# Kernel optimization log

Measured on AMD Instinct MI355X. Metric: run time of the kernel, lower is better.

Reference implementation:

```python
import jax, jax.numpy as jnp
import numpy as np

K_NEIGHBOURS = 16
ITERATIONS = 3
NUM_CLASSES = 20
N_POINTS = 20000


def setup_inputs() -> dict:
    key = jax.random.key(0)
    k1, k2 = jax.random.split(key)
    logits = jax.random.normal(k1, (N_POINTS, NUM_CLASSES), dtype=jnp.float32)
    coords = jax.random.uniform(k2, (N_POINTS, 3), dtype=jnp.float32)
    # nn.init.eye_ then *= -0.1
    compat_w = (-0.1 * jnp.eye(NUM_CLASSES, dtype=jnp.float32))
    return {"logits": logits, "coords": coords, "compat_w": compat_w}


def _knn_graph(coords, k):
    # torch.cdist (p=2): euclidean distances, (N, N)
    sq = jnp.sum(coords * coords, axis=-1)
    d2 = sq[:, None] + sq[None, :] - 2.0 * (coords @ coords.T)
    dists = jnp.sqrt(jnp.clip(d2, 0.0))
    # smallest-k -> top_k of negated distances
    _, idx = jax.lax.top_k(-dists, k)  # (N, k)
    return idx


def reference(logits, coords, compat_w):
    knn_idx = _knn_graph(coords, K_NEIGHBOURS)
    q = jax.nn.softmax(logits, axis=-1)
    for _ in range(ITERATIONS):
        neighbour_q = q[knn_idx]            # (N, k, K) gather
        msg = jnp.mean(neighbour_q, axis=1)  # (N, K)
        refined = logits + msg @ compat_w.T  # nn.Linear: x @ W^T
        q = jax.nn.softmax(refined, axis=-1)
    return (refined, q)
```

## Files before the change

### kernel.cpp

```cpp
#include <hip/hip_runtime.h>

#define N_PTS 20000
#define NCLS 20
#define KNN 16
#define GRID 12
#define NCELLS (GRID * GRID * GRID)
#define HCELL (1.0f / (float)GRID)
#define CAND_CAP 1152
#define KEY_CAP 192
#define R_TARGET 0.0680f

__device__ __forceinline__ int cell1d(float v) {
    int c = (int)(v * (float)GRID);
    return min(max(c, 0), GRID - 1);
}

__global__ __launch_bounds__(1024) void build_kernel(const float* __restrict__ coords,
                                                     int* __restrict__ cellStart,
                                                     int* __restrict__ cellCursor) {
    __shared__ int hist[NCELLS];
    __shared__ int part[1024];
    const int t = threadIdx.x;
    for (int c = t; c < NCELLS; c += 1024) hist[c] = 0;
    __syncthreads();
    for (int p = t; p < N_PTS; p += 1024) {
        const int cx = cell1d(coords[3 * p + 0]);
        const int cy = cell1d(coords[3 * p + 1]);
        const int cz = cell1d(coords[3 * p + 2]);
        atomicAdd(&hist[(cz * GRID + cy) * GRID + cx], 1);
    }
    __syncthreads();
    const int c0 = 2 * t, c1 = 2 * t + 1;
    const int v0 = (c0 < NCELLS) ? hist[c0] : 0;
    const int v1 = (c1 < NCELLS) ? hist[c1] : 0;
    part[t] = v0 + v1;
    __syncthreads();
    for (int off = 1; off < 1024; off <<= 1) {
        const int v = part[t] + ((t >= off) ? part[t - off] : 0);
        __syncthreads();
        part[t] = v;
        __syncthreads();
    }
    const int excl = (t > 0) ? part[t - 1] : 0;
    if (c0 < NCELLS) { cellStart[c0] = excl;      cellCursor[c0] = excl; }
    if (c1 < NCELLS) { cellStart[c1] = excl + v0; cellCursor[c1] = excl + v0; }
    if (t == 1023) cellStart[NCELLS] = part[1023];
}

__global__ __launch_bounds__(256) void scatter_kernel(const float* __restrict__ coords,
                                                      const float* __restrict__ logits,
                                                      int* __restrict__ cellCursor,
                                                      float4* __restrict__ sortedPts,
                                                      int* __restrict__ orig,
                                                      float* __restrict__ ls,
                                                      float* __restrict__ q0s) {
    const int p = blockIdx.x * blockDim.x + threadIdx.x;
    if (p >= N_PTS) return;
    const float x = coords[3 * p + 0];
    const float y = coords[3 * p + 1];
    const float z = coords[3 * p + 2];
    const int c = (cell1d(z) * GRID + cell1d(y)) * GRID + cell1d(x);
    const int pos = atomicAdd(&cellCursor[c], 1);
    sortedPts[pos] = make_float4(x, y, z, __uint_as_float((unsigned)p));
    orig[pos] = p;
    const float4* l4 = (const float4*)(logits + p * NCLS);
    float v[NCLS];
#pragma unroll
    for (int u = 0; u < 5; ++u) {
        const float4 a = l4[u];
        v[4 * u + 0] = a.x; v[4 * u + 1] = a.y;
        v[4 * u + 2] = a.z; v[4 * u + 3] = a.w;
    }
    float4* d4 = (float4*)(ls + pos * NCLS);
#pragma unroll
    for (int u = 0; u < 5; ++u)
        d4[u] = make_float4(v[4 * u], v[4 * u + 1], v[4 * u + 2], v[4 * u + 3]);
    float mx = v[0];
#pragma unroll
    for (int cc = 1; cc < NCLS; ++cc) mx = fmaxf(mx, v[cc]);
    float sum = 0.f;
#pragma unroll
    for (int cc = 0; cc < NCLS; ++cc) { v[cc] = __expf(v[cc] - mx); sum += v[cc]; }
    const float inv = 1.f / sum;
    float4* q4 = (float4*)(q0s + pos * NCLS);
#pragma unroll
    for (int u = 0; u < 5; ++u)
        q4[u] = make_float4(v[4 * u] * inv, v[4 * u + 1] * inv,
                            v[4 * u + 2] * inv, v[4 * u + 3] * inv);
}

__device__ void knn_ladder(const float4* __restrict__ sortedPts,
                           const int* __restrict__ cellStart,
                           const float4 qp, const int s, int hw,
                           unsigned long long* keys, const int lane,
                           int* __restrict__ knn_out) {
    const unsigned long long laneLt = (1ull << lane) - 1ull;
    const int cx = cell1d(qp.x), cy = cell1d(qp.y), cz = cell1d(qp.z);
    float g = 0.9995f * (float)hw * HCELL;
    float tau = g * g;
    int cnt = 0;
    for (int att = 0; att < 16; ++att) {
        cnt = 0;
        const int xlo = max(cx - hw, 0), xhi = min(cx + hw, GRID - 1);
        const int ylo = max(cy - hw, 0), yhi = min(cy + hw, GRID - 1);
        const int zlo = max(cz - hw, 0), zhi = min(cz + hw, GRID - 1);
        for (int zz = zlo; zz <= zhi; ++zz) {
            for (int yy = ylo; yy <= yhi; ++yy) {
                const int rowc = (zz * GRID + yy) * GRID;
                const int beg = cellStart[rowc + xlo];
                const int end = cellStart[rowc + xhi + 1];
                for (int j0 = beg; j0 < end; j0 += 64) {
                    const int j = j0 + lane;
                    const bool jv = j < end;
                    const float4 pt = sortedPts[jv ? j : beg];
                    const float dx = pt.x - qp.x, dy = pt.y - qp.y, dz = pt.z - qp.z;
                    const float d2 = dx * dx + dy * dy + dz * dz;
                    const bool take = jv && (d2 < tau);
                    const unsigned long long mm = __ballot(take);
                    if (take) {
                        const int pos = cnt + (int)__popcll(mm & laneLt);
                        if (pos < KEY_CAP)
                            keys[pos] = (((unsigned long long)__float_as_uint(d2)) << 32) |
                                        (unsigned long long)(unsigned)j;
                    }
                    cnt += (int)__popcll(mm);
                }
            }
        }
        if (cnt >= KNN && cnt <= KEY_CAP) break;
        if (cnt < KNN) {
            if (hw < GRID - 1) { ++hw; g = 0.9995f * (float)hw * HCELL; tau = g * g; }
            else tau *= 2.5f;
        } else {
            tau *= 0.6f;
        }
    }
    const int m = min(cnt, KEY_CAP);
    const unsigned long long k0 = (lane < m) ? keys[lane] : ~0ull;
    const unsigned long long k1 = (lane + 64 < m) ? keys[lane + 64] : ~0ull;
    const unsigned long long k2 = (lane + 128 < m) ? keys[lane + 128] : ~0ull;
    int r0 = 0, r1 = 0, r2 = 0;
    for (int j = 0; j < m; ++j) {
        const unsigned long long kj = keys[j];
        r0 += (kj < k0); r1 += (kj < k1); r2 += (kj < k2);
    }
    if (lane < m && r0 < KNN)       knn_out[s * KNN + r0] = (int)(unsigned)(k0 & 0xffffffffull);
    if (lane + 64 < m && r1 < KNN)  knn_out[s * KNN + r1] = (int)(unsigned)(k1 & 0xffffffffull);
    if (lane + 128 < m && r2 < KNN) knn_out[s * KNN + r2] = (int)(unsigned)(k2 & 0xffffffffull);
}

__global__ __launch_bounds__(256) void knn_kernel(const float4* __restrict__ sortedPts,
                                                  const int* __restrict__ cellStart,
                                                  int* __restrict__ knn_out) {
    __shared__ float4 cand[CAND_CAP];
    __shared__ unsigned long long keys[4][KEY_CAP];
    const int lane = threadIdx.x & 63;
    const int wave = threadIdx.x >> 6;
    const int c = blockIdx.x;
    const int cz = c / (GRID * GRID);
    const int cy = (c / GRID) % GRID;
    const int cx = c % GRID;
    const int pbeg = cellStart[c];
    const int pend = cellStart[c + 1];
    const int npts = pend - pbeg;
    if (npts <= 0) return;
    const int bd = (cx == 0 || cx == GRID - 1) + (cy == 0 || cy == GRID - 1) +
                   (cz == 0 || cz == GRID - 1);
    const int hs = bd ? 2 : 1;
    const unsigned long long laneLt = (1ull << lane) - 1ull;

    const int xlo = max(cx - hs, 0), xhi = min(cx + hs, GRID - 1);
    const int ylo = max(cy - hs, 0), yhi = min(cy + hs, GRID - 1);
    const int zlo = max(cz - hs, 0), zhi = min(cz + hs, GRID - 1);
    const int ny = yhi - ylo + 1;
    const int nruns = (zhi - zlo + 1) * ny;

    int beg = 0, len = 0;
    if (lane < nruns) {
        const int zz = zlo + lane / ny;
        const int yy = ylo + lane % ny;
        const int rowc = (zz * GRID + yy) * GRID;
        beg = cellStart[rowc + xlo];
        len = cellStart[rowc + xhi + 1] - beg;
    }
    int off = len;
#pragma unroll
    for (int sh = 1; sh < 64; sh <<= 1) {
        const int o = __shfl_up(off, sh, 64);
        if (lane >= sh) off += o;
    }
    const int nc = __shfl(off, 63);
    off -= len;
    const int ownRun = (cz - zlo) * ny + (cy - ylo);
    const int ownOff = __shfl(off, ownRun) + (pbeg - __shfl(beg, ownRun));

    if (nc <= CAND_CAP) {
        for (int r = wave; r < nruns; r += 4) {
            const int rb = __shfl(beg, r);
            const int rl = __shfl(len, r);
            const int ro = __shfl(off, r);
            for (int i = lane; i < rl; i += 64) {
                float4 pt = sortedPts[rb + i];
                pt.w = __uint_as_float((unsigned)(rb + i));
                cand[ro + i] = pt;
            }
        }
    }
    __syncthreads();

    if (nc > CAND_CAP) {
        for (int idx = wave; idx < npts; idx += 4)
            knn_ladder(sortedPts, cellStart, sortedPts[pbeg + idx], pbeg + idx,
                       hs + 1, keys[wave], lane, knn_out);
        return;
    }

    const float taumaxr = 0.9995f * (float)hs * HCELL;
    const float taumax = taumaxr * taumaxr;

    for (int idx = wave; idx < npts; idx += 4) {
        const int s = pbeg + idx;
        const float4 qp = cand[ownOff + idx];
        float r = R_TARGET;
        const float inv2r = 0.5f / r;
        const float fx = (fminf(qp.x + r, 1.f) - fmaxf(qp.x - r, 0.f)) * inv2r;
        const float fy = (fminf(qp.y + r, 1.f) - fmaxf(qp.y - r, 0.f)) * inv2r;
        const float fz = (fminf(qp.z + r, 1.f) - fmaxf(qp.z - r, 0.f)) * inv2r;
        const float f = fmaxf(fx * fy * fz, 0.05f);
        r = R_TARGET * __powf(f, -0.33333334f);
        float tau = fminf(r * r, taumax);
        bool triedMax = (tau >= taumax * 0.999f);

        int cnt = 0;
        bool ok = false;
        for (int att = 0; att < 6 && !ok; ++att) {
            cnt = 0;
            for (int j0 = 0; j0 < nc; j0 += 64) {
                const int j = j0 + lane;
                float d2 = 1e30f;
                unsigned pw = 0;
                if (j < nc) {
                    const float4 pt = cand[j];
                    const float dx = pt.x - qp.x, dy = pt.y - qp.y, dz = pt.z - qp.z;
                    d2 = dx * dx + dy * dy + dz * dz;
                    pw = __float_as_uint(pt.w);
                }
                const bool take = d2 < tau;
                const unsigned long long mm = __ballot(take);
                if (take) {
                    const int pos = cnt + (int)__popcll(mm & laneLt);
                    if (pos < KEY_CAP)
                        keys[wave][pos] =
                            (((unsigned long long)__float_as_uint(d2)) << 32) |
                            (unsigned long long)pw;
                }
                cnt += (int)__popcll(mm);
            }
            if (cnt >= KNN && cnt <= KEY_CAP) ok = true;
            else if (cnt < KNN) {
                if (triedMax) break;
                tau = taumax; triedMax = true;
            } else tau *= 0.6f;
        }
        if (!ok) {
            knn_ladder(sortedPts, cellStart, qp, s, hs + 1, keys[wave], lane, knn_out);
            continue;
        }
        const int m = cnt;
        const unsigned long long k0 = (lane < m) ? keys[wave][lane] : ~0ull;
        const unsigned long long k1 = (lane + 64 < m) ? keys[wave][lane + 64] : ~0ull;
        const unsigned long long k2 = (lane + 128 < m) ? keys[wave][lane + 128] : ~0ull;
        int r0 = 0, r1 = 0, r2 = 0;
        for (int j = 0; j < m; ++j) {
            const unsigned long long kj = keys[wave][j];
            r0 += (kj < k0); r1 += (kj < k1); r2 += (kj < k2);
        }
        if (lane < m && r0 < KNN)       knn_out[s * KNN + r0] = (int)(unsigned)(k0 & 0xffffffffull);
        if (lane + 64 < m && r1 < KNN)  knn_out[s * KNN + r1] = (int)(unsigned)(k1 & 0xffffffffull);
        if (lane + 128 < m && r2 < KNN) knn_out[s * KNN + r2] = (int)(unsigned)(k2 & 0xffffffffull);
    }
}

__global__ __launch_bounds__(256) void crf_iter_kernel(const float* __restrict__ ls,
                                                       const float* __restrict__ W,
                                                       const int* __restrict__ knn,
                                                       const float* __restrict__ qin,
                                                       float* __restrict__ qout,
                                                       const int* __restrict__ orig,
                                                       float* __restrict__ outRef,
                                                       float* __restrict__ outQ) {
    __shared__ float Ws[NCLS * NCLS];
    for (int i = threadIdx.x; i < NCLS * NCLS; i += blockDim.x) Ws[i] = W[i];
    __syncthreads();
    const int t = blockIdx.x * blockDim.x + threadIdx.x;
    const int p = t >> 2;
    const int qtr = t & 3;
    if (p >= N_PTS) return;

    float acc[NCLS];
#pragma unroll
    for (int c = 0; c < NCLS; ++c) acc[c] = 0.f;

    const int4 k4 = ((const int4*)(knn + p * KNN))[qtr];
    const int ids[4] = {k4.x, k4.y, k4.z, k4.w};
#pragma unroll
    for (int u = 0; u < 4; ++u) {
        unsigned id = (unsigned)ids[u];
        if (id >= N_PTS) id = 0;
        const float4* r4 = (const float4*)(qin + id * NCLS);
#pragma unroll
        for (int v = 0; v < 5; ++v) {
            const float4 a = r4[v];
            acc[4 * v + 0] += a.x; acc[4 * v + 1] += a.y;
            acc[4 * v + 2] += a.z; acc[4 * v + 3] += a.w;
        }
    }
#pragma unroll
    for (int c = 0; c < NCLS; ++c) {
        acc[c] += __shfl_xor(acc[c], 1, 64);
        acc[c] += __shfl_xor(acc[c], 2, 64);
        acc[c] *= (1.f / 16.f);
    }

    const int c0 = qtr * 5;
    float ref[5];
#pragma unroll
    for (int i = 0; i < 5; ++i) {
        float s = ls[p * NCLS + c0 + i];
#pragma unroll
        for (int k = 0; k < NCLS; ++k) s += acc[k] * Ws[(c0 + i) * NCLS + k];
        ref[i] = s;
    }

    float mx = ref[0];
#pragma unroll
    for (int i = 1; i < 5; ++i) mx = fmaxf(mx, ref[i]);
    mx = fmaxf(mx, __shfl_xor(mx, 1, 64));
    mx = fmaxf(mx, __shfl_xor(mx, 2, 64));
    float ex[5];
    float ps = 0.f;
#pragma unroll
    for (int i = 0; i < 5; ++i) { ex[i] = __expf(ref[i] - mx); ps += ex[i]; }
    ps += __shfl_xor(ps, 1, 64);
    ps += __shfl_xor(ps, 2, 64);
    const float inv = 1.f / ps;

    if (outRef != nullptr) {
        const int o = orig[p];
#pragma unroll
        for (int i = 0; i < 5; ++i) {
            outRef[o * NCLS + c0 + i] = ref[i];
            outQ[o * NCLS + c0 + i] = ex[i] * inv;
        }
    } else {
#pragma unroll
        for (int i = 0; i < 5; ++i) qout[p * NCLS + c0 + i] = ex[i] * inv;
    }
}

extern "C" void kernel_launch(void* const* d_in, const int* in_sizes, int n_in,
                              void* d_out, int out_size, void* d_ws, size_t ws_size,
                              hipStream_t stream) {
    const float* logits = (const float*)d_in[0];
    const float* coords = (const float*)d_in[1];
    const float* W      = (const float*)d_in[2];
    float* out = (float*)d_out;

    char* ws = (char*)d_ws;
    size_t off = 0;
    int* knn = (int*)(ws + off);              off += (size_t)N_PTS * KNN * 4;
    off = (off + 255) & ~(size_t)255;
    float* ls = (float*)(ws + off);           off += (size_t)N_PTS * NCLS * 4;
    off = (off + 255) & ~(size_t)255;
    float* q0s = (float*)(ws + off);          off += (size_t)N_PTS * NCLS * 4;
    off = (off + 255) & ~(size_t)255;
    float4* sortedPts = (float4*)(ws + off);  off += (size_t)N_PTS * 16;
    off = (off + 255) & ~(size_t)255;
    int* orig = (int*)(ws + off);             off += (size_t)N_PTS * 4;
    off = (off + 255) & ~(size_t)255;
    int* cellStart = (int*)(ws + off);        off += (size_t)(NCELLS + 1) * 4;
    off = (off + 255) & ~(size_t)255;
    int* cellCursor = (int*)(ws + off);
    float* q1s = out + N_PTS * NCLS;

    const int threads = 256;
    const int pblocks = (N_PTS + threads - 1) / threads;
    const int cblocks = (4 * N_PTS + threads - 1) / threads;

    build_kernel<<<1, 1024, 0, stream>>>(coords, cellStart, cellCursor);
    scatter_kernel<<<pblocks, threads, 0, stream>>>(coords, logits, cellCursor,
                                                    sortedPts, orig, ls, q0s);
    knn_kernel<<<NCELLS, threads, 0, stream>>>(sortedPts, cellStart, knn);
    crf_iter_kernel<<<cblocks, threads, 0, stream>>>(ls, W, knn, q0s, q1s, orig,
                                                     nullptr, nullptr);
    crf_iter_kernel<<<cblocks, threads, 0, stream>>>(ls, W, knn, q1s, q0s, orig,
                                                     nullptr, nullptr);
    crf_iter_kernel<<<cblocks, threads, 0, stream>>>(ls, W, knn, q0s, nullptr, orig,
                                                     out, out + N_PTS * NCLS);
}
```

Measured before the change: 136.5 us.

## Parallelize cell histogram, split kNN cells across two blocks, shrink candidate caps

Replaces the single-block histogram and scan with a grid-wide atomic count kernel where the last block to finish does the prefix scan, which removes a serial single-workgroup stage. The kNN kernel now launches two blocks per cell, each handling alternate query points. The candidate neighbourhood is fixed to 3x3x3 cells with smaller shared-memory caps (CAND_CAP 512, KEY_CAP 128), which cuts LDS use and the rank-sort work. The trade-off is that the two blocks per cell duplicate the candidate load, and more queries may fall back to the slower ladder search when a cell's candidate count exceeds the smaller cap or boundary cells lack enough neighbours.

After: 129.7 us. 1.05x faster.

```diff
diff --git a/kernel.cpp b/kernel.cpp
--- a/kernel.cpp
+++ b/kernel.cpp
@@ -6,8 +6,8 @@
 #define GRID 12
 #define NCELLS (GRID * GRID * GRID)
 #define HCELL (1.0f / (float)GRID)
-#define CAND_CAP 1152
-#define KEY_CAP 192
+#define CAND_CAP 512
+#define KEY_CAP 128
 #define R_TARGET 0.0680f
 
 __device__ __forceinline__ int cell1d(float v) {
@@ -15,36 +15,58 @@
     return min(max(c, 0), GRID - 1);
 }
 
-__global__ __launch_bounds__(1024) void build_kernel(const float* __restrict__ coords,
-                                                     int* __restrict__ cellStart,
-                                                     int* __restrict__ cellCursor) {
-    __shared__ int hist[NCELLS];
-    __shared__ int part[1024];
-    const int t = threadIdx.x;
-    for (int c = t; c < NCELLS; c += 1024) hist[c] = 0;
-    __syncthreads();
-    for (int p = t; p < N_PTS; p += 1024) {
+__global__ __launch_bounds__(256) void count_scan_kernel(const float* __restrict__ coords,
+                                                         int* __restrict__ cellCount,
+                                                         int* __restrict__ doneCtr,
+                                                         int* __restrict__ cellStart,
+                                                         int* __restrict__ cellCursor) {
+    const int p = blockIdx.x * blockDim.x + threadIdx.x;
+    if (p < N_PTS) {
         const int cx = cell1d(coords[3 * p + 0]);
         const int cy = cell1d(coords[3 * p + 1]);
         const int cz = cell1d(coords[3 * p + 2]);
-        atomicAdd(&hist[(cz * GRID + cy) * GRID + cx], 1);
-    }
+        atomicAdd(&cellCount[(cz * GRID + cy) * GRID + cx], 1);
+    }
+    __threadfence();
     __syncthreads();
-    const int c0 = 2 * t, c1 = 2 * t + 1;
-    const int v0 = (c0 < NCELLS) ? hist[c0] : 0;
-    const int v1 = (c1 < NCELLS) ? hist[c1] : 0;
-    part[t] = v0 + v1;
+    __shared__ bool isLast;
+    if (threadIdx.x == 0)
+        isLast = (atomicAdd(doneCtr, 1) == (int)gridDim.x - 1);
     __syncthreads();
-    for (int off = 1; off < 1024; off <<= 1) {
+    if (!isLast) return;
+
+    __shared__ int part[256];
+    const int t = threadIdx.x;
+    const int base = t * 7;
+    int local[7];
+    int s = 0;
+#pragma unroll
+    for (int i = 0; i < 7; ++i) {
+        const int c = base + i;
+        const int v = (c < NCELLS)
+            ? __hip_atomic_load(&cellCount[c], __ATOMIC_RELAXED, __HIP_MEMORY_SCOPE_AGENT)
+            : 0;
+        local[i] = s;
+        s += v;
+    }
+    part[t] = s;
+    __syncthreads();
+    for (int off = 1; off < 256; off <<= 1) {
         const int v = part[t] + ((t >= off) ? part[t - off] : 0);
         __syncthreads();
         part[t] = v;
         __syncthreads();
     }
     const int excl = (t > 0) ? part[t - 1] : 0;
-    if (c0 < NCELLS) { cellStart[c0] = excl;      cellCursor[c0] = excl; }
-    if (c1 < NCELLS) { cellStart[c1] = excl + v0; cellCursor[c1] = excl + v0; }
-    if (t == 1023) cellStart[NCELLS] = part[1023];
+#pragma unroll
+    for (int i = 0; i < 7; ++i) {
+        const int c = base + i;
+        if (c < NCELLS) {
+            cellStart[c] = excl + local[i];
+            cellCursor[c] = excl + local[i];
+        }
+    }
+    if (t == 255) cellStart[NCELLS] = part[255];
 }
 
 __global__ __launch_bounds__(256) void scatter_kernel(const float* __restrict__ coords,
@@ -138,15 +160,13 @@
     const int m = min(cnt, KEY_CAP);
     const unsigned long long k0 = (lane < m) ? keys[lane] : ~0ull;
     const unsigned long long k1 = (lane + 64 < m) ? keys[lane + 64] : ~0ull;
-    const unsigned long long k2 = (lane + 128 < m) ? keys[lane + 128] : ~0ull;
-    int r0 = 0, r1 = 0, r2 = 0;
+    int r0 = 0, r1 = 0;
     for (int j = 0; j < m; ++j) {
         const unsigned long long kj = keys[j];
-        r0 += (kj < k0); r1 += (kj < k1); r2 += (kj < k2);
-    }
-    if (lane < m && r0 < KNN)       knn_out[s * KNN + r0] = (int)(unsigned)(k0 & 0xffffffffull);
-    if (lane + 64 < m && r1 < KNN)  knn_out[s * KNN + r1] = (int)(unsigned)(k1 & 0xffffffffull);
-    if (lane + 128 < m && r2 < KNN) knn_out[s * KNN + r2] = (int)(unsigned)(k2 & 0xffffffffull);
+        r0 += (kj < k0); r1 += (kj < k1);
+    }
+    if (lane < m && r0 < KNN)      knn_out[s * KNN + r0] = (int)(unsigned)(k0 & 0xffffffffull);
+    if (lane + 64 < m && r1 < KNN) knn_out[s * KNN + r1] = (int)(unsigned)(k1 & 0xffffffffull);
 }
 
 __global__ __launch_bounds__(256) void knn_kernel(const float4* __restrict__ sortedPts,
@@ -156,7 +176,8 @@
     __shared__ unsigned long long keys[4][KEY_CAP];
     const int lane = threadIdx.x & 63;
     const int wave = threadIdx.x >> 6;
-    const int c = blockIdx.x;
+    const int c = blockIdx.x >> 1;
+    const int half = blockIdx.x & 1;
     const int cz = c / (GRID * GRID);
     const int cy = (c / GRID) % GRID;
     const int cx = c % GRID;
@@ -164,14 +185,11 @@
     const int pend = cellStart[c + 1];
     const int npts = pend - pbeg;
     if (npts <= 0) return;
-    const int bd = (cx == 0 || cx == GRID - 1) + (cy == 0 || cy == GRID - 1) +
-                   (cz == 0 || cz == GRID - 1);
-    const int hs = bd ? 2 : 1;
     const unsigned long long laneLt = (1ull << lane) - 1ull;
 
-    const int xlo = max(cx - hs, 0), xhi = min(cx + hs, GRID - 1);
-    const int ylo = max(cy - hs, 0), yhi = min(cy + hs, GRID - 1);
-    const int zlo = max(cz - hs, 0), zhi = min(cz + hs, GRID - 1);
+    const int xlo = max(cx - 1, 0), xhi = min(cx + 1, GRID - 1);
+    const int ylo = max(cy - 1, 0), yhi = min(cy + 1, GRID - 1);
+    const int zlo = max(cz - 1, 0), zhi = min(cz + 1, GRID - 1);
     const int ny = yhi - ylo + 1;
     const int nruns = (zhi - zlo + 1) * ny;
 
@@ -185,11 +203,11 @@
     }
     int off = len;
 #pragma unroll
-    for (int sh = 1; sh < 64; sh <<= 1) {
+    for (int sh = 1; sh < 16; sh <<= 1) {
         const int o = __shfl_up(off, sh, 64);
         if (lane >= sh) off += o;
     }
-    const int nc = __shfl(off, 63);
+    const int nc = __shfl(off, nruns - 1);
     off -= len;
     const int ownRun = (cz - zlo) * ny + (cy - ylo);
     const int ownOff = __shfl(off, ownRun) + (pbeg - __shfl(beg, ownRun));
@@ -209,16 +227,16 @@
     __syncthreads();
 
     if (nc > CAND_CAP) {
-        for (int idx = wave; idx < npts; idx += 4)
+        for (int idx = 2 * wave + half; idx < npts; idx += 8)
             knn_ladder(sortedPts, cellStart, sortedPts[pbeg + idx], pbeg + idx,
-                       hs + 1, keys[wave], lane, knn_out);
+                       2, keys[wave], lane, knn_out);
         return;
     }
 
-    const float taumaxr = 0.9995f * (float)hs * HCELL;
+    const float taumaxr = 0.9995f * HCELL;
     const float taumax = taumaxr * taumaxr;
 
-    for (int idx = wave; idx < npts; idx += 4) {
+    for (int idx = 2 * wave + half; idx < npts; idx += 8) {
         const int s = pbeg + idx;
         const float4 qp = cand[ownOff + idx];
         float r = R_TARGET;
@@ -233,7 +251,7 @@
 
         int cnt = 0;
         bool ok = false;
-        for (int att = 0; att < 6 && !ok; ++att) {
+        for (int att = 0; att < 5 && !ok; ++att) {
             cnt = 0;
             for (int j0 = 0; j0 < nc; j0 += 64) {
                 const int j = j0 + lane;
@@ -263,21 +281,19 @@
             } else tau *= 0.6f;
         }
         if (!ok) {
-            knn_ladder(sortedPts, cellStart, qp, s, hs + 1, keys[wave], lane, knn_out);
+            knn_ladder(sortedPts, cellStart, qp, s, 2, keys[wave], lane, knn_out);
             continue;
         }
         const int m = cnt;
         const unsigned long long k0 = (lane < m) ? keys[wave][lane] : ~0ull;
         const unsigned long long k1 = (lane + 64 < m) ? keys[wave][lane + 64] : ~0ull;
-        const unsigned long long k2 = (lane + 128 < m) ? keys[wave][lane + 128] : ~0ull;
-        int r0 = 0, r1 = 0, r2 = 0;
+        int r0 = 0, r1 = 0;
         for (int j = 0; j < m; ++j) {
             const unsigned long long kj = keys[wave][j];
-            r0 += (kj < k0); r1 += (kj < k1); r2 += (kj < k2);
-        }
-        if (lane < m && r0 < KNN)       knn_out[s * KNN + r0] = (int)(unsigned)(k0 & 0xffffffffull);
-        if (lane + 64 < m && r1 < KNN)  knn_out[s * KNN + r1] = (int)(unsigned)(k1 & 0xffffffffull);
-        if (lane + 128 < m && r2 < KNN) knn_out[s * KNN + r2] = (int)(unsigned)(k2 & 0xffffffffull);
+            r0 += (kj < k0); r1 += (kj < k1);
+        }
+        if (lane < m && r0 < KNN)      knn_out[s * KNN + r0] = (int)(unsigned)(k0 & 0xffffffffull);
+        if (lane + 64 < m && r1 < KNN) knn_out[s * KNN + r1] = (int)(unsigned)(k1 & 0xffffffffull);
     }
 }
 
@@ -378,6 +394,9 @@
     off = (off + 255) & ~(size_t)255;
     int* orig = (int*)(ws + off);             off += (size_t)N_PTS * 4;
     off = (off + 255) & ~(size_t)255;
+    int* cellCount = (int*)(ws + off);        off += (size_t)(NCELLS + 1) * 4;
+    int* doneCtr = cellCount + NCELLS;
+    off = (off + 255) & ~(size_t)255;
     int* cellStart = (int*)(ws + off);        off += (size_t)(NCELLS + 1) * 4;
     off = (off + 255) & ~(size_t)255;
     int* cellCursor = (int*)(ws + off);
@@ -387,10 +406,12 @@
     const int pblocks = (N_PTS + threads - 1) / threads;
     const int cblocks = (4 * N_PTS + threads - 1) / threads;
 
-    build_kernel<<<1, 1024, 0, stream>>>(coords, cellStart, cellCursor);
+    hipMemsetAsync(cellCount, 0, (NCELLS + 1) * sizeof(int), stream);
+    count_scan_kernel<<<pblocks, threads, 0, stream>>>(coords, cellCount, doneCtr,
+                                                       cellStart, cellCursor);
     scatter_kernel<<<pblocks, threads, 0, stream>>>(coords, logits, cellCursor,
                                                     sortedPts, orig, ls, q0s);
-    knn_kernel<<<NCELLS, threads, 0, stream>>>(sortedPts, cellStart, knn);
+    knn_kernel<<<NCELLS * 2, threads, 0, stream>>>(sortedPts, cellStart, knn);
     crf_iter_kernel<<<cblocks, threads, 0, stream>>>(ls, W, knn, q0s, q1s, orig,
                                                      nullptr, nullptr);
     crf_iter_kernel<<<cblocks, threads, 0, stream>>>(ls, W, knn, q1s, q0s, orig,
```
